# Optimization experiments

Hardware: AMD Instinct MI355X
Metric: run time of the kernel (lower is better)

Reference implementation:

```python
import jax, jax.numpy as jnp
import numpy as np

B, S, D, H = 2, 2048, 2048, 16
HD = D // H          # head dim 128
R = 64               # qk_rope_head_dim
LR = 64              # kv_low_rank_dim
FF = 2048            # ffn_dim per expert
E = 8                # num routed experts
K = 2                # top_k
ROPE_BASE = 10000.0
LN_EPS = 1e-5


def setup_inputs() -> dict:
    key = jax.random.key(0)
    ks = jax.random.split(key, 20)
    def rn(k, shape, fan_in):
        return jax.random.normal(k, shape, jnp.float32) * (1.0 / np.sqrt(fan_in))
    return {
        "hidden_states": jax.random.normal(ks[0], (B, S, D), jnp.float32),
        "position_ids": jnp.arange(S, dtype=jnp.int32)[None, :],
        # attention projections, stored [in, out]
        "Wq": rn(ks[1], (D, D), D), "Wk": rn(ks[2], (D, D), D), "Wv": rn(ks[3], (D, D), D),
        "Wkc": rn(ks[4], (HD, LR), HD), "Wvc": rn(ks[5], (HD, LR), HD),
        "Wqa": rn(ks[6], (HD, LR), HD), "Wqg": rn(ks[7], (HD, HD), HD),
        "Wov": rn(ks[8], (LR, HD), LR), "Wo": rn(ks[9], (D, D), D),
        "ln1_w": jnp.ones((D,), jnp.float32), "ln1_b": jnp.zeros((D,), jnp.float32),
        "ln2_w": jnp.ones((D,), jnp.float32), "ln2_b": jnp.zeros((D,), jnp.float32),
        # MoE
        "Wg": rn(ks[10], (D, E), D),
        "We1": rn(ks[11], (E, D, FF), D), "We2": rn(ks[12], (E, FF, D), FF), "We3": rn(ks[13], (E, D, FF), D),
        "Ws1": rn(ks[14], (D, FF), D), "Ws2": rn(ks[15], (FF, D), FF), "Ws3": rn(ks[16], (D, FF), D),
    }


def _layernorm(x, w, b):
    mu = jnp.mean(x, -1, keepdims=True)
    var = jnp.mean(jnp.square(x - mu), -1, keepdims=True)
    return (x - mu) * jax.lax.rsqrt(var + LN_EPS) * w + b


def _rotate_half(x):
    h = x.shape[-1] // 2
    return jnp.concatenate([-x[..., h:], x[..., :h]], axis=-1)


def _rope_cos_sin(position_ids, dtype):
    inv_freq = 1.0 / (ROPE_BASE ** (jnp.arange(0, R, 2, dtype=jnp.float32) / R))
    t = jnp.arange(S, dtype=jnp.float32)
    freqs = t[:, None] * inv_freq[None, :]           # [S, R/2]
    emb = jnp.concatenate([freqs, freqs], -1)        # [S, R]
    cos = jnp.cos(emb).astype(dtype)[position_ids][:, :, None, :]  # [1,S,1,R]
    sin = jnp.sin(emb).astype(dtype)[position_ids][:, :, None, :]
    return cos, sin


def reference(hidden_states, position_ids, Wq, Wk, Wv, Wkc, Wvc, Wqa, Wqg, Wov, Wo,
              ln1_w, ln1_b, ln2_w, ln2_b, Wg, We1, We2, We3, Ws1, Ws2, Ws3):
    x = _layernorm(hidden_states, ln1_w, ln1_b)
    # ---- MLA attention ----
    q = (x @ Wq).reshape(B, S, H, HD)
    k = (x @ Wk).reshape(B, S, H, HD)
    v = (x @ Wv).reshape(B, S, H, HD)
    cos, sin = _rope_cos_sin(position_ids, x.dtype)
    qr = q[..., :R] * cos + _rotate_half(q[..., :R]) * sin
    kr = k[..., :R] * cos + _rotate_half(k[..., :R]) * sin
    q = jnp.concatenate([qr, q[..., R:]], -1)
    k = jnp.concatenate([kr, k[..., R:]], -1)
    k_c = k @ Wkc                                   # [B,S,H,LR]
    v_c = v @ Wvc                                   # [B,S,H,LR]
    q_a = q @ Wqa                                   # [B,S,H,LR]
    q_gate = q @ Wqg                                # [B,S,H,HD]
    scores = jnp.einsum('bqhr,bkhr->bhqk', q_a, k_c) / np.sqrt(LR)
    attw = jax.nn.softmax(scores.astype(jnp.float32), axis=-1).astype(q.dtype)
    att_c = jnp.einsum('bhqk,bkhr->bqhr', attw, v_c)  # [B,S,H,LR]
    uplift = att_c @ Wov                              # [B,S,H,HD]
    gated = (jax.nn.silu(q_gate) * uplift).reshape(B, S, D)
    attn_out = gated @ Wo
    h = hidden_states + attn_out
    # ---- MoE with shared expert ----
    xf = _layernorm(h, ln2_w, ln2_b).reshape(-1, D)   # [T, D]
    shared = (jax.nn.silu(xf @ Ws1) * (xf @ Ws3)) @ Ws2
    logits = xf @ Wg                                  # [T, E]
    probs = jax.nn.softmax(logits.astype(jnp.float32), axis=-1)
    topw, topi = jax.lax.top_k(probs, K)
    topw = topw / jnp.sum(topw, -1, keepdims=True)
    T = xf.shape[0]
    combine = jnp.zeros((T, E), xf.dtype).at[jnp.arange(T)[:, None], topi].set(topw.astype(xf.dtype))
    h1 = jnp.einsum('td,edf->etf', xf, We1)
    h3 = jnp.einsum('td,edf->etf', xf, We3)
    eout = jnp.einsum('etf,efd->etd', jax.nn.silu(h1) * h3, We2)
    moe = shared + jnp.einsum('te,etd->td', combine, eout)
    return h + moe.reshape(B, S, D)
```

## Files before the change

kernel.cpp:

```cpp
#include <hip/hip_runtime.h>
#include <math.h>

typedef __bf16 bf16;
typedef __bf16 bf16x8 __attribute__((ext_vector_type(8)));
typedef float f32x4 __attribute__((ext_vector_type(4)));

#define B_ 2
#define S_ 2048
#define D_ 2048
#define H_ 16
#define FF_ 2048
#define E_ 8
#define T_ 4096
#define TH_ 65536
#define CAP_ 4096

#define MFMA_(a, b, c) __builtin_amdgcn_mfma_f32_16x16x32_bf16(a, b, c, 0, 0, 0)

__device__ __forceinline__ int swz(int row, int byteoff) {
  return row * 128 + (byteoff ^ ((row & 7) << 4));
}
__device__ __forceinline__ int swzf(int row, int byteoff) {
  return row * 256 + (byteoff ^ ((row & 7) << 5));
}

__device__ __forceinline__ void split2(float x, bf16& h, bf16& m) {
  h = (bf16)x;
  m = (bf16)(x - (float)h);
}

__device__ __forceinline__ void frag_split(const char* p, int off, bf16x8& r0, bf16x8& r1) {
  f32x4 u = *(const f32x4*)(p + off);
  f32x4 v = *(const f32x4*)(p + off + 16);
#pragma unroll
  for (int j = 0; j < 4; j++) { bf16 a, b; split2(u[j], a, b); r0[j] = a; r1[j] = b; }
#pragma unroll
  for (int j = 0; j < 4; j++) { bf16 a, b; split2(v[j], a, b); r0[4 + j] = a; r1[4 + j] = b; }
}

__device__ __forceinline__ f32x4 dot3(bf16x8 a0, bf16x8 a1,
                                      bf16x8 b0, bf16x8 b1, f32x4 c) {
  c = MFMA_(a0, b0, c);
  c = MFMA_(a0, b1, c);
  c = MFMA_(a1, b0, c);
  return c;
}

__device__ __forceinline__ float blk_sum(float v, float* sbuf, int tid) {
#pragma unroll
  for (int mk = 32; mk; mk >>= 1) v += __shfl_xor(v, mk);
  __syncthreads();
  if ((tid & 63) == 0) sbuf[tid >> 6] = v;
  __syncthreads();
  return sbuf[0] + sbuf[1] + sbuf[2] + sbuf[3];
}

__global__ __launch_bounds__(256) void k_transpose(const float* __restrict__ src,
                                                   bf16* __restrict__ dst, int R, int C) {
  __shared__ float tile[32][33];
  int tx = threadIdx.x, ty = threadIdx.y;
  int c0 = blockIdx.x * 32, r0 = blockIdx.y * 32;
#pragma unroll
  for (int j = 0; j < 32; j += 8) tile[ty + j][tx] = src[(size_t)(r0 + ty + j) * C + (c0 + tx)];
  __syncthreads();
#pragma unroll
  for (int j = 0; j < 32; j += 8)
    dst[(size_t)(c0 + ty + j) * R + (r0 + tx)] = (bf16)tile[tx][ty + j];
}

__global__ __launch_bounds__(256) void k_transpose32(const float* __restrict__ src,
                                                     float* __restrict__ dst, int R, int C) {
  __shared__ float tile[32][33];
  int tx = threadIdx.x, ty = threadIdx.y;
  int c0 = blockIdx.x * 32, r0 = blockIdx.y * 32;
#pragma unroll
  for (int j = 0; j < 32; j += 8) tile[ty + j][tx] = src[(size_t)(r0 + ty + j) * C + (c0 + tx)];
  __syncthreads();
#pragma unroll
  for (int j = 0; j < 32; j += 8)
    dst[(size_t)(c0 + ty + j) * R + (r0 + tx)] = tile[tx][ty + j];
}

template <int MODE>
__global__ __launch_bounds__(256) void k_transpose_moe(const float* __restrict__ W1,
                                                       const float* __restrict__ W3,
                                                       bf16* __restrict__ dstB, int eBase) {
  __shared__ float tile[32][33];
  int tx = threadIdx.x, ty = threadIdx.y;
  int z = blockIdx.z;
  const float* src;
  if (MODE == 0) src = ((z & 1) ? W3 : W1) + (size_t)(eBase + (z >> 1)) * 4194304;
  else src = W1 + (size_t)(eBase + z) * 4194304;
  bf16* dst = dstB + (size_t)z * 4194304;
  int c0 = blockIdx.x * 32, r0 = blockIdx.y * 32;
#pragma unroll
  for (int j = 0; j < 32; j += 8) tile[ty + j][tx] = src[(size_t)(r0 + ty + j) * 2048 + (c0 + tx)];
  __syncthreads();
#pragma unroll
  for (int j = 0; j < 32; j += 8)
    dst[(size_t)(c0 + ty + j) * 2048 + (r0 + tx)] = (bf16)tile[tx][ty + j];
}

__global__ __launch_bounds__(256) void k_transpose_split(const float* __restrict__ src,
                                                         bf16* __restrict__ dh, bf16* __restrict__ dl,
                                                         int R, int C) {
  __shared__ float tile[32][33];
  int tx = threadIdx.x, ty = threadIdx.y;
  int c0 = blockIdx.x * 32, r0 = blockIdx.y * 32;
#pragma unroll
  for (int j = 0; j < 32; j += 8) tile[ty + j][tx] = src[(size_t)(r0 + ty + j) * C + (c0 + tx)];
  __syncthreads();
#pragma unroll
  for (int j = 0; j < 32; j += 8) {
    float v = tile[tx][ty + j];
    bf16 h, l;
    split2(v, h, l);
    size_t o = (size_t)(c0 + ty + j) * R + (r0 + tx);
    dh[o] = h;
    dl[o] = l;
  }
}

__global__ __launch_bounds__(256) void k_tr_v32s(const float* __restrict__ vc,
                                                 bf16* __restrict__ vh, bf16* __restrict__ vl) {
  __shared__ float tile[32][33];
  int tx = threadIdx.x, ty = threadIdx.y;
  int z = blockIdx.z;
  int s0 = blockIdx.x * 32, r0 = blockIdx.y * 32;
  int b = z >> 4, h = z & 15;
#pragma unroll
  for (int j = 0; j < 32; j += 8) {
    int s = s0 + ty + j;
    tile[ty + j][tx] = vc[((size_t)((b * S_ + s) * H_ + h)) * 64 + r0 + tx];
  }
  __syncthreads();
#pragma unroll
  for (int j = 0; j < 32; j += 8) {
    int r = r0 + ty + j;
    float v = tile[tx][ty + j];
    bf16 hh, ll;
    split2(v, hh, ll);
    size_t o = ((size_t)(z * 64 + r)) * S_ + s0 + tx;
    vh[o] = hh;
    vl[o] = ll;
  }
}

__global__ __launch_bounds__(256) void k_ln32_split(const float* __restrict__ x, const float* __restrict__ w,
                                                    const float* __restrict__ bb,
                                                    bf16* __restrict__ oh, bf16* __restrict__ ol) {
  __shared__ float sbuf[4];
  int row = blockIdx.x, tid = threadIdx.x;
  const float* xr = x + (size_t)row * D_;
  float v[8];
  float s = 0.f;
#pragma unroll
  for (int j = 0; j < 8; j++) { v[j] = xr[tid + 256 * j]; s += v[j]; }
  float mu = blk_sum(s, sbuf, tid) * (1.f / D_);
  float qs = 0.f;
#pragma unroll
  for (int j = 0; j < 8; j++) { float d = v[j] - mu; qs += d * d; }
  float rs = rsqrtf(blk_sum(qs, sbuf, tid) * (1.f / D_) + 1e-5f);
#pragma unroll
  for (int j = 0; j < 8; j++) {
    int c = tid + 256 * j;
    float xn = (v[j] - mu) * rs * w[c] + bb[c];
    bf16 h, l;
    split2(xn, h, l);
    oh[(size_t)row * D_ + c] = h;
    ol[(size_t)row * D_ + c] = l;
  }
}

template <int EPI>
__global__ __launch_bounds__(256) void k_gemm32s(const bf16* __restrict__ Ah, const bf16* __restrict__ Al, int lda,
                                                 const bf16* __restrict__ Bh, const bf16* __restrict__ Bl, int ldb,
                                                 float* __restrict__ C, int ldc,
                                                 int M, int N, int Kd,
                                                 const float* __restrict__ resid) {
  __shared__ __align__(16) char Ahs[16384];
  __shared__ __align__(16) char Als[16384];
  __shared__ __align__(16) char Bhs[16384];
  __shared__ __align__(16) char Bls[16384];
  int bm = blockIdx.y * 128, bn = blockIdx.x * 128;
  int tid = threadIdx.x;
  int srow = tid >> 3, scol = (tid & 7) * 8;
  int arow[4], brow[4];
#pragma unroll
  for (int i = 0; i < 4; i++) {
    int r = bm + srow + 32 * i;
    arow[i] = r < M ? r : (M - 1);
    int q = bn + srow + 32 * i;
    brow[i] = q < N ? q : (N - 1);
  }
  f32x4 acc[4][4] = {};
  int lane = tid & 63, w = tid >> 6, g = lane >> 4, lr = lane & 15;
  int wm = (w >> 1) * 64, wn = (w & 1) * 64;
  for (int kt = 0; kt < Kd; kt += 64) {
#pragma unroll
    for (int i = 0; i < 4; i++) {
      int o = swz(srow + 32 * i, scol * 2);
      *(uint4*)(Ahs + o) = *(const uint4*)(Ah + (size_t)arow[i] * lda + kt + scol);
      *(uint4*)(Als + o) = *(const uint4*)(Al + (size_t)arow[i] * lda + kt + scol);
      *(uint4*)(Bhs + o) = *(const uint4*)(Bh + (size_t)brow[i] * ldb + kt + scol);
      *(uint4*)(Bls + o) = *(const uint4*)(Bl + (size_t)brow[i] * ldb + kt + scol);
    }
    __syncthreads();
#pragma unroll
    for (int ks = 0; ks < 2; ks++) {
      bf16x8 ah[4], al[4], bh[4], bl[4];
#pragma unroll
      for (int m = 0; m < 4; m++) {
        ah[m] = *(const bf16x8*)(Ahs + swz(wm + m * 16 + lr, ks * 64 + g * 16));
        al[m] = *(const bf16x8*)(Als + swz(wm + m * 16 + lr, ks * 64 + g * 16));
      }
#pragma unroll
      for (int n = 0; n < 4; n++) {
        bh[n] = *(const bf16x8*)(Bhs + swz(wn + n * 16 + lr, ks * 64 + g * 16));
        bl[n] = *(const bf16x8*)(Bls + swz(wn + n * 16 + lr, ks * 64 + g * 16));
      }
#pragma unroll
      for (int m = 0; m < 4; m++)
#pragma unroll
        for (int n = 0; n < 4; n++)
          acc[m][n] = dot3(ah[m], al[m], bh[n], bl[n], acc[m][n]);
    }
    __syncthreads();
  }
#pragma unroll
  for (int m = 0; m < 4; m++)
#pragma unroll
    for (int n = 0; n < 4; n++)
#pragma unroll
      for (int r = 0; r < 4; r++) {
        int row = bm + wm + m * 16 + g * 4 + r;
        int col = bn + wn + n * 16 + lr;
        if (row < M && col < N) {
          float val = acc[m][n][r];
          if (EPI == 1) val += resid[(size_t)row * ldc + col];
          C[(size_t)row * ldc + col] = val;
        }
      }
}

template <int EPI>
__global__ __launch_bounds__(256) void k_gemm32(const float* __restrict__ A, int lda,
                                                const float* __restrict__ Bt, int ldb,
                                                float* __restrict__ C, int ldc,
                                                int M, int N, int Kd,
                                                bf16* __restrict__ Ch, bf16* __restrict__ Cl) {
  __shared__ __align__(16) char As[32768];
  __shared__ __align__(16) char Bs[32768];
  int bm = blockIdx.y * 128, bn = blockIdx.x * 128;
  int tid = threadIdx.x;
  int srow = tid >> 3, scol = (tid & 7) * 8;
  int arow[4], brow[4];
#pragma unroll
  for (int i = 0; i < 4; i++) {
    int r = bm + srow + 32 * i;
    arow[i] = r < M ? r : (M - 1);
    int q = bn + srow + 32 * i;
    brow[i] = q < N ? q : (N - 1);
  }
  f32x4 acc[4][4] = {};
  int lane = tid & 63, w = tid >> 6, g = lane >> 4, lr = lane & 15;
  int wm = (w >> 1) * 64, wn = (w & 1) * 64;
  for (int kt = 0; kt < Kd; kt += 64) {
#pragma unroll
    for (int i = 0; i < 4; i++) {
      const float* pa = A + (size_t)arow[i] * lda + kt + scol;
      f32x4 va0 = *(const f32x4*)pa, va1 = *(const f32x4*)(pa + 4);
      const float* pb = Bt + (size_t)brow[i] * ldb + kt + scol;
      f32x4 vb0 = *(const f32x4*)pb, vb1 = *(const f32x4*)(pb + 4);
      int o = swzf(srow + 32 * i, scol * 4);
      *(f32x4*)(As + o) = va0;
      *(f32x4*)(As + o + 16) = va1;
      *(f32x4*)(Bs + o) = vb0;
      *(f32x4*)(Bs + o + 16) = vb1;
    }
    __syncthreads();
#pragma unroll
    for (int ks = 0; ks < 2; ks++) {
      bf16x8 a0[4], a1[4], b0[4], b1[4];
#pragma unroll
      for (int m = 0; m < 4; m++)
        frag_split(As, swzf(wm + m * 16 + lr, ks * 128 + g * 32), a0[m], a1[m]);
#pragma unroll
      for (int n = 0; n < 4; n++)
        frag_split(Bs, swzf(wn + n * 16 + lr, ks * 128 + g * 32), b0[n], b1[n]);
#pragma unroll
      for (int m = 0; m < 4; m++)
#pragma unroll
        for (int n = 0; n < 4; n++)
          acc[m][n] = dot3(a0[m], a1[m], b0[n], b1[n], acc[m][n]);
    }
    __syncthreads();
  }
#pragma unroll
  for (int m = 0; m < 4; m++)
#pragma unroll
    for (int n = 0; n < 4; n++)
#pragma unroll
      for (int r = 0; r < 4; r++) {
        int row = bm + wm + m * 16 + g * 4 + r;
        int col = bn + wn + n * 16 + lr;
        if (row < M && col < N) {
          float val = acc[m][n][r];
          if (EPI == 2) {
            bf16 h, l;
            split2(val, h, l);
            Ch[(size_t)row * ldc + col] = h;
            Cl[(size_t)row * ldc + col] = l;
          } else {
            C[(size_t)row * ldc + col] = val;
          }
        }
      }
}

__global__ __launch_bounds__(256) void k_rope32(float* __restrict__ q, float* __restrict__ k) {
  int idx = blockIdx.x * 256 + threadIdx.x;
  int i = idx & 31, rowth = idx >> 5;
  int s = (rowth >> 4) & (S_ - 1);
  size_t base = (size_t)rowth * 128;
  float freq = expf(-0.28782313662425576f * (float)i);
  float ang = (float)s * freq;
  float sn, cs;
  sincosf(ang, &sn, &cs);
  float q1 = q[base + i], q2 = q[base + i + 32];
  q[base + i] = q1 * cs - q2 * sn;
  q[base + i + 32] = q2 * cs + q1 * sn;
  float k1 = k[base + i], k2 = k[base + i + 32];
  k[base + i] = k1 * cs - k2 * sn;
  k[base + i + 32] = k2 * cs + k1 * sn;
}

__global__ __launch_bounds__(256) void k_attn32p(const bf16* __restrict__ qh, const bf16* __restrict__ ql,
                                                 const bf16* __restrict__ kh, const bf16* __restrict__ kl,
                                                 const bf16* __restrict__ vh, const bf16* __restrict__ vl,
                                                 float* __restrict__ attc) {
  __shared__ __align__(16) char L[65536];
  int qt = blockIdx.x, bh = blockIdx.y;
  int b = bh >> 4, h = bh & 15;
  int tid = threadIdx.x, lane = tid & 63, w = tid >> 6, g = lane >> 4, lr = lane & 15;
  int s0 = qt * 128;
  int srow = tid >> 3, scol = (tid & 7) * 8;
  char* Qsh = L;
  char* Qsl = L + 16384;
#pragma unroll
  for (int i = 0; i < 4; i++) {
    int row = srow + 32 * i;
    size_t goff = ((size_t)((b * S_ + s0 + row) * H_ + h)) * 64 + scol;
    int o = swz(row, scol * 2);
    *(uint4*)(Qsh + o) = *(const uint4*)(qh + goff);
    *(uint4*)(Qsl + o) = *(const uint4*)(ql + goff);
  }
  __syncthreads();
  bf16x8 qf0[2][2], qf1[2][2];
#pragma unroll
  for (int m = 0; m < 2; m++)
#pragma unroll
    for (int ks = 0; ks < 2; ks++) {
      qf0[m][ks] = *(const bf16x8*)(Qsh + swz(w * 32 + m * 16 + lr, ks * 64 + g * 16));
      qf1[m][ks] = *(const bf16x8*)(Qsl + swz(w * 32 + m * 16 + lr, ks * 64 + g * 16));
    }
  __syncthreads();
  char* Ksh = L;
  char* Ksl = L + 8192;
  char* Vsh = L + 16384;
  char* Vsl = L + 24576;
  char* Ph = L + 32768 + w * 8192;
  char* Pl = Ph + 4096;
  f32x4 acc[2][4] = {};
  float mrun[2][4], lrun[2][4];
#pragma unroll
  for (int m = 0; m < 2; m++)
#pragma unroll
    for (int r = 0; r < 4; r++) { mrun[m][r] = -1e30f; lrun[m][r] = 0.f; }
  for (int kt = 0; kt < S_; kt += 64) {
#pragma unroll
    for (int i = 0; i < 2; i++) {
      int rr = srow + 32 * i;
      size_t koff = ((size_t)((b * S_ + kt + rr) * H_ + h)) * 64 + scol;
      size_t voff = ((size_t)(bh * 64 + rr)) * S_ + kt + scol;
      int o = swz(rr, scol * 2);
      *(uint4*)(Ksh + o) = *(const uint4*)(kh + koff);
      *(uint4*)(Ksl + o) = *(const uint4*)(kl + koff);
      *(uint4*)(Vsh + o) = *(const uint4*)(vh + voff);
      *(uint4*)(Vsl + o) = *(const uint4*)(vl + voff);
    }
    __syncthreads();
    f32x4 sc[2][4] = {};
#pragma unroll
    for (int ks = 0; ks < 2; ks++) {
      bf16x8 k0[4], k1[4];
#pragma unroll
      for (int n = 0; n < 4; n++) {
        k0[n] = *(const bf16x8*)(Ksh + swz(n * 16 + lr, ks * 64 + g * 16));
        k1[n] = *(const bf16x8*)(Ksl + swz(n * 16 + lr, ks * 64 + g * 16));
      }
#pragma unroll
      for (int m = 0; m < 2; m++)
#pragma unroll
        for (int n = 0; n < 4; n++)
          sc[m][n] = dot3(qf0[m][ks], qf1[m][ks], k0[n], k1[n], sc[m][n]);
    }
#pragma unroll
    for (int m = 0; m < 2; m++)
#pragma unroll
      for (int r = 0; r < 4; r++) {
        float a0 = sc[m][0][r] * 0.125f, a1 = sc[m][1][r] * 0.125f;
        float a2 = sc[m][2][r] * 0.125f, a3 = sc[m][3][r] * 0.125f;
        float mx = fmaxf(fmaxf(a0, a1), fmaxf(a2, a3));
#pragma unroll
        for (int mk = 1; mk < 16; mk <<= 1) mx = fmaxf(mx, __shfl_xor(mx, mk));
        float mo = mrun[m][r];
        float mn = fmaxf(mo, mx);
        float f = expf(mo - mn);
        float p0 = expf(a0 - mn), p1 = expf(a1 - mn), p2 = expf(a2 - mn), p3 = expf(a3 - mn);
        int prow = m * 16 + g * 4 + r;
        bf16 h0, l0, h1, l1, h2, l2, h3, l3;
        split2(p0, h0, l0);
        split2(p1, h1, l1);
        split2(p2, h2, l2);
        split2(p3, h3, l3);
        *(bf16*)(Ph + swz(prow, lr * 2)) = h0;
        *(bf16*)(Pl + swz(prow, lr * 2)) = l0;
        *(bf16*)(Ph + swz(prow, 32 + lr * 2)) = h1;
        *(bf16*)(Pl + swz(prow, 32 + lr * 2)) = l1;
        *(bf16*)(Ph + swz(prow, 64 + lr * 2)) = h2;
        *(bf16*)(Pl + swz(prow, 64 + lr * 2)) = l2;
        *(bf16*)(Ph + swz(prow, 96 + lr * 2)) = h3;
        *(bf16*)(Pl + swz(prow, 96 + lr * 2)) = l3;
        float ps = p0 + p1 + p2 + p3;
#pragma unroll
        for (int mk = 1; mk < 16; mk <<= 1) ps += __shfl_xor(ps, mk);
        lrun[m][r] = lrun[m][r] * f + ps;
        mrun[m][r] = mn;
#pragma unroll
        for (int n = 0; n < 4; n++) acc[m][n][r] *= f;
      }
#pragma unroll
    for (int ks = 0; ks < 2; ks++) {
      bf16x8 p0f[2], p1f[2], v0f[4], v1f[4];
#pragma unroll
      for (int m = 0; m < 2; m++) {
        p0f[m] = *(const bf16x8*)(Ph + swz(m * 16 + lr, ks * 64 + g * 16));
        p1f[m] = *(const bf16x8*)(Pl + swz(m * 16 + lr, ks * 64 + g * 16));
      }
#pragma unroll
      for (int n = 0; n < 4; n++) {
        v0f[n] = *(const bf16x8*)(Vsh + swz(n * 16 + lr, ks * 64 + g * 16));
        v1f[n] = *(const bf16x8*)(Vsl + swz(n * 16 + lr, ks * 64 + g * 16));
      }
#pragma unroll
      for (int m = 0; m < 2; m++)
#pragma unroll
        for (int n = 0; n < 4; n++)
          acc[m][n] = dot3(p0f[m], p1f[m], v0f[n], v1f[n], acc[m][n]);
    }
    __syncthreads();
  }
#pragma unroll
  for (int m = 0; m < 2; m++)
#pragma unroll
    for (int n = 0; n < 4; n++)
#pragma unroll
      for (int r = 0; r < 4; r++) {
        int s = s0 + w * 32 + m * 16 + g * 4 + r;
        attc[((size_t)((b * S_ + s) * H_ + h)) * 64 + n * 16 + lr] = acc[m][n][r] / lrun[m][r];
      }
}

__global__ __launch_bounds__(256) void k_silu32_split(const float* __restrict__ a, const float* __restrict__ b,
                                                      bf16* __restrict__ ch, bf16* __restrict__ cl, long n) {
  long i = ((long)blockIdx.x * 256 + threadIdx.x) * 8;
  if (i >= n) return;
  f32x4 av0 = *(const f32x4*)(a + i), av1 = *(const f32x4*)(a + i + 4);
  f32x4 bv0 = *(const f32x4*)(b + i), bv1 = *(const f32x4*)(b + i + 4);
  bf16x8 hv, lv;
#pragma unroll
  for (int j = 0; j < 4; j++) {
    float x = av0[j];
    float g = x / (1.f + expf(-x)) * bv0[j];
    bf16 h, l;
    split2(g, h, l);
    hv[j] = h; lv[j] = l;
  }
#pragma unroll
  for (int j = 0; j < 4; j++) {
    float x = av1[j];
    float g = x / (1.f + expf(-x)) * bv1[j];
    bf16 h, l;
    split2(g, h, l);
    hv[4 + j] = h; lv[4 + j] = l;
  }
  *(bf16x8*)(ch + i) = hv;
  *(bf16x8*)(cl + i) = lv;
}

__global__ __launch_bounds__(256) void k_router(const float* __restrict__ hbuf,
                                                const float* __restrict__ w2, const float* __restrict__ b2,
                                                const float* __restrict__ Wg, bf16* __restrict__ xf,
                                                int* __restrict__ count, int* __restrict__ permg,
                                                int* __restrict__ permt, float* __restrict__ wslot) {
  __shared__ float sbuf[4];
  int t = blockIdx.x, tid = threadIdx.x;
  const float* hr = hbuf + (size_t)t * D_;
  float v[8];
  float s = 0.f;
#pragma unroll
  for (int j = 0; j < 8; j++) { v[j] = hr[tid + 256 * j]; s += v[j]; }
  float mu = blk_sum(s, sbuf, tid) * (1.f / D_);
  float qs = 0.f;
#pragma unroll
  for (int j = 0; j < 8; j++) { float d = v[j] - mu; qs += d * d; }
  float rs = rsqrtf(blk_sum(qs, sbuf, tid) * (1.f / D_) + 1e-5f);
  float le[8] = {0, 0, 0, 0, 0, 0, 0, 0};
#pragma unroll
  for (int j = 0; j < 8; j++) {
    int c = tid + 256 * j;
    float xn = (v[j] - mu) * rs * w2[c] + b2[c];
    xf[(size_t)t * D_ + c] = (bf16)xn;
    const float* wr = Wg + (size_t)c * 8;
#pragma unroll
    for (int e = 0; e < 8; e++) le[e] += xn * wr[e];
  }
#pragma unroll
  for (int e = 0; e < 8; e++) le[e] = blk_sum(le[e], sbuf, tid);
  if (tid == 0) {
    float mx = le[0];
    for (int e = 1; e < 8; e++) mx = fmaxf(mx, le[e]);
    float p[8], sum = 0.f;
    for (int e = 0; e < 8; e++) { p[e] = expf(le[e] - mx); sum += p[e]; }
    int i0 = 0;
    for (int e = 1; e < 8; e++) if (p[e] > p[i0]) i0 = e;
    int i1 = (i0 == 0) ? 1 : 0;
    for (int e = 0; e < 8; e++) if (e != i0 && p[e] > p[i1]) i1 = e;
    float inv = 1.f / (p[i0] + p[i1]);
    int pos0 = atomicAdd(&count[i0], 1);
    permg[i0 * CAP_ + pos0] = 2 * t;
    permt[i0 * CAP_ + pos0] = t;
    int pos1 = atomicAdd(&count[i1], 1);
    permg[i1 * CAP_ + pos1] = 2 * t + 1;
    permt[i1 * CAP_ + pos1] = t;
    wslot[2 * t] = p[i0] * inv;
    wslot[2 * t + 1] = p[i1] * inv;
  }
}

template <bool GATHER>
__global__ __launch_bounds__(256) void k_gemm(const bf16* __restrict__ A, int lda,
                                              const bf16* __restrict__ Bt, int ldb,
                                              bf16* __restrict__ C, int ldc, int M, int N, int Kd,
                                              const int* __restrict__ amap,
                                              const int* __restrict__ cmap,
                                              const int* __restrict__ countp) {
  int Mz = countp ? countp[0] : M;
  int bm = blockIdx.y * 128, bn = blockIdx.x * 128;
  if (bm >= Mz) return;
  __shared__ __align__(16) char As[16384];
  __shared__ __align__(16) char Bs[16384];
  int tid = threadIdx.x;
  int srow = tid >> 3, scol = (tid & 7) * 8;
  int arow[4], brow[4];
#pragma unroll
  for (int i = 0; i < 4; i++) {
    int r = bm + srow + 32 * i;
    if (GATHER) { int rc = r < Mz ? r : (Mz - 1); arow[i] = amap[rc]; }
    else { arow[i] = r < M ? r : (M - 1); }
    int bq = bn + srow + 32 * i;
    brow[i] = bq < N ? bq : (N - 1);
  }
  f32x4 acc[4][4] = {};
  int lane = tid & 63, w = tid >> 6, g = lane >> 4, lr = lane & 15;
  int wm = (w >> 1) * 64, wn = (w & 1) * 64;
  for (int kt = 0; kt < Kd; kt += 64) {
#pragma unroll
    for (int i = 0; i < 4; i++) {
      uint4 da = *(const uint4*)(A + (size_t)arow[i] * lda + kt + scol);
      *(uint4*)(As + swz(srow + 32 * i, scol * 2)) = da;
      uint4 db = *(const uint4*)(Bt + (size_t)brow[i] * ldb + kt + scol);
      *(uint4*)(Bs + swz(srow + 32 * i, scol * 2)) = db;
    }
    __syncthreads();
#pragma unroll
    for (int ks = 0; ks < 2; ks++) {
      bf16x8 af[4], bfr[4];
#pragma unroll
      for (int m = 0; m < 4; m++) af[m] = *(const bf16x8*)(As + swz(wm + m * 16 + lr, ks * 64 + g * 16));
#pragma unroll
      for (int n = 0; n < 4; n++) bfr[n] = *(const bf16x8*)(Bs + swz(wn + n * 16 + lr, ks * 64 + g * 16));
#pragma unroll
      for (int m = 0; m < 4; m++)
#pragma unroll
        for (int n = 0; n < 4; n++)
          acc[m][n] = MFMA_(af[m], bfr[n], acc[m][n]);
    }
    __syncthreads();
  }
#pragma unroll
  for (int m = 0; m < 4; m++)
#pragma unroll
    for (int n = 0; n < 4; n++)
#pragma unroll
      for (int r = 0; r < 4; r++) {
        int row = bm + wm + m * 16 + g * 4 + r;
        int col = bn + wn + n * 16 + lr;
        if (row < Mz && col < N) {
          size_t orow = cmap ? (size_t)cmap[row] : (size_t)row;
          C[orow * ldc + col] = (bf16)acc[m][n][r];
        }
      }
}

template <int MODE>
__global__ __launch_bounds__(256) void k_gemm_moe(const bf16* __restrict__ A, int lda,
                                                  const bf16* __restrict__ wteB,
                                                  bf16* __restrict__ C0, bf16* __restrict__ C1, int ldc,
                                                  int N, int Kd,
                                                  const int* __restrict__ permt, const int* __restrict__ permg,
                                                  const int* __restrict__ count, int eBase) {
  int z = blockIdx.z;
  int e;
  const int* amap;
  const int* cmap;
  bf16* C;
  if (MODE == 0) {
    e = eBase + (z >> 1);
    amap = permt + e * CAP_;
    cmap = permg + e * CAP_;
    C = (z & 1) ? C1 : C0;
  } else {
    e = eBase + z;
    amap = permg + e * CAP_;
    cmap = permg + e * CAP_;
    C = C0;
  }
  const bf16* Bt = wteB + (size_t)z * 4194304;
  int Mz = count[e];
  int bm = blockIdx.y * 128, bn = blockIdx.x * 128;
  if (bm >= Mz) return;
  __shared__ __align__(16) char As[16384];
  __shared__ __align__(16) char Bs[16384];
  int tid = threadIdx.x;
  int srow = tid >> 3, scol = (tid & 7) * 8;
  int arow[4], brow[4];
#pragma unroll
  for (int i = 0; i < 4; i++) {
    int r = bm + srow + 32 * i;
    int rc = r < Mz ? r : (Mz - 1);
    arow[i] = amap[rc];
    int bq = bn + srow + 32 * i;
    brow[i] = bq < N ? bq : (N - 1);
  }
  f32x4 acc[4][4] = {};
  int lane = tid & 63, w = tid >> 6, g = lane >> 4, lr = lane & 15;
  int wm = (w >> 1) * 64, wn = (w & 1) * 64;
  for (int kt = 0; kt < Kd; kt += 64) {
#pragma unroll
    for (int i = 0; i < 4; i++) {
      uint4 da = *(const uint4*)(A + (size_t)arow[i] * lda + kt + scol);
      *(uint4*)(As + swz(srow + 32 * i, scol * 2)) = da;
      uint4 db = *(const uint4*)(Bt + (size_t)brow[i] * 2048 + kt + scol);
      *(uint4*)(Bs + swz(srow + 32 * i, scol * 2)) = db;
    }
    __syncthreads();
#pragma unroll
    for (int ks = 0; ks < 2; ks++) {
      bf16x8 af[4], bfr[4];
#pragma unroll
      for (int m = 0; m < 4; m++) af[m] = *(const bf16x8*)(As + swz(wm + m * 16 + lr, ks * 64 + g * 16));
#pragma unroll
      for (int n = 0; n < 4; n++) bfr[n] = *(const bf16x8*)(Bs + swz(wn + n * 16 + lr, ks * 64 + g * 16));
#pragma unroll
      for (int m = 0; m < 4; m++)
#pragma unroll
        for (int n = 0; n < 4; n++)
          acc[m][n] = MFMA_(af[m], bfr[n], acc[m][n]);
    }
    __syncthreads();
  }
#pragma unroll
  for (int m = 0; m < 4; m++)
#pragma unroll
    for (int n = 0; n < 4; n++)
#pragma unroll
      for (int r = 0; r < 4; r++) {
        int row = bm + wm + m * 16 + g * 4 + r;
        int col = bn + wn + n * 16 + lr;
        if (row < Mz && col < N) {
          C[(size_t)cmap[row] * ldc + col] = (bf16)acc[m][n][r];
        }
      }
}

__global__ __launch_bounds__(256) void k_silu_mul(const bf16* __restrict__ a, const bf16* __restrict__ b,
                                                  bf16* __restrict__ c, long n) {
  long i = ((long)blockIdx.x * 256 + threadIdx.x) * 8;
  if (i >= n) return;
  bf16x8 av = *(const bf16x8*)(a + i);
  bf16x8 bv = *(const bf16x8*)(b + i);
  bf16x8 cv;
#pragma unroll
  for (int j = 0; j < 8; j++) {
    float x = (float)av[j];
    float y = (float)bv[j];
    cv[j] = (bf16)(x / (1.f + expf(-x)) * y);
  }
  *(bf16x8*)(c + i) = cv;
}

__global__ __launch_bounds__(256) void k_combine(const float* __restrict__ hbuf, const bf16* __restrict__ shr,
                                                 const bf16* __restrict__ eout, const float* __restrict__ wslot,
                                                 float* __restrict__ out) {
  long i = ((long)blockIdx.x * 256 + threadIdx.x) * 4;
  int t = (int)(i >> 11);
  int c = (int)(i & (D_ - 1));
  float w0 = wslot[2 * t], w1 = wslot[2 * t + 1];
  float4 hv = *(const float4*)(hbuf + i);
  const bf16* s4 = shr + i;
  const bf16* e0 = eout + ((size_t)(2 * t)) * D_ + c;
  const bf16* e1 = e0 + D_;
  float4 o;
  o.x = hv.x + (float)s4[0] + w0 * (float)e0[0] + w1 * (float)e1[0];
  o.y = hv.y + (float)s4[1] + w0 * (float)e0[1] + w1 * (float)e1[1];
  o.z = hv.z + (float)s4[2] + w0 * (float)e0[2] + w1 * (float)e1[2];
  o.w = hv.w + (float)s4[3] + w0 * (float)e0[3] + w1 * (float)e1[3];
  *(float4*)(out + i) = o;
}

extern "C" void kernel_launch(void* const* d_in, const int* in_sizes, int n_in, void* d_out,
                              int out_size, void* d_ws, size_t ws_size, hipStream_t stream) {
  const float* hidden = (const float*)d_in[0];
  const float* Wq = (const float*)d_in[2];
  const float* Wk = (const float*)d_in[3];
  const float* Wv = (const float*)d_in[4];
  const float* Wkc = (const float*)d_in[5];
  const float* Wvc = (const float*)d_in[6];
  const float* Wqa = (const float*)d_in[7];
  const float* Wqg = (const float*)d_in[8];
  const float* Wov = (const float*)d_in[9];
  const float* Wo = (const float*)d_in[10];
  const float* ln1w = (const float*)d_in[11];
  const float* ln1b = (const float*)d_in[12];
  const float* ln2w = (const float*)d_in[13];
  const float* ln2b = (const float*)d_in[14];
  const float* Wg = (const float*)d_in[15];
  const float* We1 = (const float*)d_in[16];
  const float* We2 = (const float*)d_in[17];
  const float* We3 = (const float*)d_in[18];
  const float* Ws1 = (const float*)d_in[19];
  const float* Ws2 = (const float*)d_in[20];
  const float* Ws3 = (const float*)d_in[21];
  float* out = (float*)d_out;
  (void)in_sizes; (void)n_in; (void)out_size;

  const size_t MB = 1ull << 20;
  char* base = (char*)d_ws;
  float* hbuf = (float*)(base);
  bf16* shr = (bf16*)(base + 32 * MB);
  int* count = (int*)(base + 48 * MB);
  int* permg = (int*)(base + 48 * MB + 4096);
  int* permt = (int*)(base + 48 * MB + 4096 + 131072);
  float* wslot = (float*)(base + 48 * MB + 4096 + 262144);
  float* wtqa32 = (float*)(base + 49 * MB);
  float* wtkc32 = (float*)(base + 49 * MB + 32768);
  float* wtvc32 = (float*)(base + 49 * MB + 65536);
  float* wtov32 = (float*)(base + 49 * MB + 98304);
  float* wtqg32 = (float*)(base + 49 * MB + 131072);
  char* A0p = base + 50 * MB;
  char* A1p = base + 82 * MB;
  char* A2p = base + 114 * MB;
  char* A3p = base + 146 * MB;
  char* A4p = base + 178 * MB;
  char* A5p = base + 210 * MB;
  if (ws_size < 242 * MB) return;

  bf16* xln_h = (bf16*)A0p;
  bf16* xln_l = (bf16*)(A0p + 16 * MB);
  bf16* wtq_h = (bf16*)A1p;
  bf16* wtq_l = (bf16*)(A1p + 8 * MB);
  bf16* wtk_h = (bf16*)(A1p + 16 * MB);
  bf16* wtk_l = (bf16*)(A1p + 24 * MB);
  bf16* wtv_h = (bf16*)A2p;
  bf16* wtv_l = (bf16*)(A2p + 8 * MB);
  float* qb = (float*)A3p;
  float* kb = (float*)A4p;
  float* vb = (float*)A5p;
  bf16* qab_h = (bf16*)A1p;
  bf16* qab_l = (bf16*)(A1p + 8 * MB);
  bf16* kcb_h = (bf16*)(A1p + 16 * MB);
  bf16* kcb_l = (bf16*)(A1p + 24 * MB);
  float* vcb = (float*)A2p;
  bf16* vct_h = (bf16*)(A2p + 16 * MB);
  bf16* vct_l = (bf16*)(A2p + 24 * MB);
  float* qgate = (float*)A0p;
  float* attc = (float*)A3p;
  bf16* wto_h = (bf16*)(A3p + 16 * MB);
  bf16* wto_l = (bf16*)(A3p + 24 * MB);
  float* uplift = (float*)A4p;
  bf16* gated_h = (bf16*)A5p;
  bf16* gated_l = (bf16*)(A5p + 16 * MB);
  bf16* xf = (bf16*)A1p;
  bf16* s1 = (bf16*)(A1p + 16 * MB);
  bf16* wts1 = (bf16*)A2p;
  bf16* wts3 = (bf16*)(A2p + 8 * MB);
  bf16* wts2 = (bf16*)(A2p + 16 * MB);
  bf16* s3 = (bf16*)A3p;
  bf16* wteB = (bf16*)A2p;
  bf16* mid1 = (bf16*)A4p;
  bf16* mid3 = (bf16*)A5p;
  bf16* midg = (bf16*)A0p;
  bf16* eout = (bf16*)A3p;

  hipMemsetAsync(count, 0, 256, stream);

  dim3 tb(32, 8);
  k_transpose_split<<<dim3(64, 64, 1), tb, 0, stream>>>(Wq, wtq_h, wtq_l, 2048, 2048);
  k_transpose_split<<<dim3(64, 64, 1), tb, 0, stream>>>(Wk, wtk_h, wtk_l, 2048, 2048);
  k_transpose_split<<<dim3(64, 64, 1), tb, 0, stream>>>(Wv, wtv_h, wtv_l, 2048, 2048);
  k_transpose32<<<dim3(2, 4, 1), tb, 0, stream>>>(Wqa, wtqa32, 128, 64);
  k_transpose32<<<dim3(2, 4, 1), tb, 0, stream>>>(Wkc, wtkc32, 128, 64);
  k_transpose32<<<dim3(2, 4, 1), tb, 0, stream>>>(Wvc, wtvc32, 128, 64);
  k_transpose32<<<dim3(4, 4, 1), tb, 0, stream>>>(Wqg, wtqg32, 128, 128);
  k_transpose32<<<dim3(4, 2, 1), tb, 0, stream>>>(Wov, wtov32, 64, 128);

  k_ln32_split<<<T_, 256, 0, stream>>>(hidden, ln1w, ln1b, xln_h, xln_l);

  k_gemm32s<0><<<dim3(16, 32, 1), 256, 0, stream>>>(xln_h, xln_l, 2048, wtq_h, wtq_l, 2048, qb, 2048, T_, 2048, 2048, nullptr);
  k_gemm32s<0><<<dim3(16, 32, 1), 256, 0, stream>>>(xln_h, xln_l, 2048, wtk_h, wtk_l, 2048, kb, 2048, T_, 2048, 2048, nullptr);
  k_gemm32s<0><<<dim3(16, 32, 1), 256, 0, stream>>>(xln_h, xln_l, 2048, wtv_h, wtv_l, 2048, vb, 2048, T_, 2048, 2048, nullptr);

  k_rope32<<<8192, 256, 0, stream>>>(qb, kb);

  k_gemm32<2><<<dim3(1, 512, 1), 256, 0, stream>>>(qb, 128, wtqa32, 128, nullptr, 64, TH_, 64, 128, qab_h, qab_l);
  k_gemm32<2><<<dim3(1, 512, 1), 256, 0, stream>>>(kb, 128, wtkc32, 128, nullptr, 64, TH_, 64, 128, kcb_h, kcb_l);
  k_gemm32<0><<<dim3(1, 512, 1), 256, 0, stream>>>(vb, 128, wtvc32, 128, vcb, 64, TH_, 64, 128, nullptr, nullptr);
  k_gemm32<0><<<dim3(1, 512, 1), 256, 0, stream>>>(qb, 128, wtqg32, 128, qgate, 128, TH_, 128, 128, nullptr, nullptr);

  k_tr_v32s<<<dim3(64, 2, 32), tb, 0, stream>>>(vcb, vct_h, vct_l);
  k_transpose_split<<<dim3(64, 64, 1), tb, 0, stream>>>(Wo, wto_h, wto_l, 2048, 2048);

  k_attn32p<<<dim3(16, 32, 1), 256, 0, stream>>>(qab_h, qab_l, kcb_h, kcb_l, vct_h, vct_l, attc);

  k_transpose<<<dim3(64, 64, 1), tb, 0, stream>>>(Ws1, wts1, 2048, 2048);
  k_transpose<<<dim3(64, 64, 1), tb, 0, stream>>>(Ws3, wts3, 2048, 2048);
  k_transpose<<<dim3(64, 64, 1), tb, 0, stream>>>(Ws2, wts2, 2048, 2048);

  k_gemm32<0><<<dim3(1, 512, 1), 256, 0, stream>>>(attc, 64, wtov32, 64, uplift, 128, TH_, 128, 64, nullptr, nullptr);
  k_silu32_split<<<4096, 256, 0, stream>>>(qgate, uplift, gated_h, gated_l, (long)TH_ * 128);
  k_gemm32s<1><<<dim3(16, 32, 1), 256, 0, stream>>>(gated_h, gated_l, 2048, wto_h, wto_l, 2048, hbuf, 2048, T_, 2048, 2048, hidden);

  k_router<<<T_, 256, 0, stream>>>(hbuf, ln2w, ln2b, Wg, xf, count, permg, permt, wslot);

  k_gemm<false><<<dim3(16, 32, 1), 256, 0, stream>>>(xf, 2048, wts1, 2048, s1, 2048, T_, 2048, 2048, nullptr, nullptr, nullptr);
  k_gemm<false><<<dim3(16, 32, 1), 256, 0, stream>>>(xf, 2048, wts3, 2048, s3, 2048, T_, 2048, 2048, nullptr, nullptr, nullptr);
  k_silu_mul<<<4096, 256, 0, stream>>>(s1, s3, s1, (long)T_ * 2048);
  k_gemm<false><<<dim3(16, 32, 1), 256, 0, stream>>>(s1, 2048, wts2, 2048, shr, 2048, T_, 2048, 2048, nullptr, nullptr, nullptr);

  for (int p = 0; p < 4; p++) {
    k_transpose_moe<0><<<dim3(64, 64, 4), tb, 0, stream>>>(We1, We3, wteB, 2 * p);
    k_gemm_moe<0><<<dim3(16, 32, 4), 256, 0, stream>>>(xf, 2048, wteB, mid1, mid3, 2048, 2048, 2048, permt, permg, count, 2 * p);
  }
  k_silu_mul<<<8192, 256, 0, stream>>>(mid1, mid3, midg, (long)2 * T_ * 2048);
  for (int q = 0; q < 2; q++) {
    k_transpose_moe<1><<<dim3(64, 64, 4), tb, 0, stream>>>(We2, nullptr, wteB, 4 * q);
    k_gemm_moe<1><<<dim3(16, 32, 4), 256, 0, stream>>>(midg, 2048, wteB, eout, nullptr, 2048, 2048, 2048, permt, permg, count, 4 * q);
  }

  k_combine<<<8192, 256, 0, stream>>>(hbuf, shr, eout, wslot, out);
}
```

Before: 1.754 ms.

## Batch same-shape launches via grid z and prioritize MFMA in attention

Folds the separate transpose and GEMM launches for Q/K/V weights, the low-rank projections and the shared-expert weights into single launches indexed by blockIdx.z. The MoE expert transposes and GEMMs now cover more experts per launch. This cuts launch count and raises per-launch parallelism, especially for the small N=64 projections. It also adds s_setprio around the MFMA loops in attention and removes the generic boundary checks in the fused QKV GEMM. The trade-off is larger workspace buffers and code specialized to fixed shapes.

```diff
diff --git a/kernel.cpp b/kernel.cpp
--- a/kernel.cpp
+++ b/kernel.cpp
@@ -55,19 +55,6 @@
   return sbuf[0] + sbuf[1] + sbuf[2] + sbuf[3];
 }
 
-__global__ __launch_bounds__(256) void k_transpose(const float* __restrict__ src,
-                                                   bf16* __restrict__ dst, int R, int C) {
-  __shared__ float tile[32][33];
-  int tx = threadIdx.x, ty = threadIdx.y;
-  int c0 = blockIdx.x * 32, r0 = blockIdx.y * 32;
-#pragma unroll
-  for (int j = 0; j < 32; j += 8) tile[ty + j][tx] = src[(size_t)(r0 + ty + j) * C + (c0 + tx)];
-  __syncthreads();
-#pragma unroll
-  for (int j = 0; j < 32; j += 8)
-    dst[(size_t)(c0 + ty + j) * R + (r0 + tx)] = (bf16)tile[tx][ty + j];
-}
-
 __global__ __launch_bounds__(256) void k_transpose32(const float* __restrict__ src,
                                                      float* __restrict__ dst, int R, int C) {
   __shared__ float tile[32][33];
@@ -79,6 +66,42 @@
 #pragma unroll
   for (int j = 0; j < 32; j += 8)
     dst[(size_t)(c0 + ty + j) * R + (r0 + tx)] = tile[tx][ty + j];
+}
+
+__global__ __launch_bounds__(256) void k_transpose32b3(const float* __restrict__ s0,
+                                                       const float* __restrict__ s1x,
+                                                       const float* __restrict__ s2,
+                                                       float* __restrict__ dbase) {
+  __shared__ float tile[32][33];
+  int z = blockIdx.z;
+  const float* src = z == 0 ? s0 : (z == 1 ? s1x : s2);
+  float* dst = dbase + (size_t)z * 8192;
+  int tx = threadIdx.x, ty = threadIdx.y;
+  int c0 = blockIdx.x * 32, r0 = blockIdx.y * 32;
+#pragma unroll
+  for (int j = 0; j < 32; j += 8) tile[ty + j][tx] = src[(size_t)(r0 + ty + j) * 64 + (c0 + tx)];
+  __syncthreads();
+#pragma unroll
+  for (int j = 0; j < 32; j += 8)
+    dst[(size_t)(c0 + ty + j) * 128 + (r0 + tx)] = tile[tx][ty + j];
+}
+
+__global__ __launch_bounds__(256) void k_transpose_sh3(const float* __restrict__ s0,
+                                                       const float* __restrict__ s1x,
+                                                       const float* __restrict__ s2,
+                                                       bf16* __restrict__ dbase) {
+  __shared__ float tile[32][33];
+  int z = blockIdx.z;
+  const float* src = z == 0 ? s0 : (z == 1 ? s1x : s2);
+  bf16* dst = dbase + (size_t)z * 4194304;
+  int tx = threadIdx.x, ty = threadIdx.y;
+  int c0 = blockIdx.x * 32, r0 = blockIdx.y * 32;
+#pragma unroll
+  for (int j = 0; j < 32; j += 8) tile[ty + j][tx] = src[(size_t)(r0 + ty + j) * 2048 + (c0 + tx)];
+  __syncthreads();
+#pragma unroll
+  for (int j = 0; j < 32; j += 8)
+    dst[(size_t)(c0 + ty + j) * 2048 + (r0 + tx)] = (bf16)tile[tx][ty + j];
 }
 
 template <int MODE>
@@ -116,6 +139,31 @@
     bf16 h, l;
     split2(v, h, l);
     size_t o = (size_t)(c0 + ty + j) * R + (r0 + tx);
+    dh[o] = h;
+    dl[o] = l;
+  }
+}
+
+__global__ __launch_bounds__(256) void k_transpose_split3(const float* __restrict__ s0,
+                                                          const float* __restrict__ s1x,
+                                                          const float* __restrict__ s2,
+                                                          bf16* __restrict__ dbase) {
+  __shared__ float tile[32][33];
+  int z = blockIdx.z;
+  const float* src = z == 0 ? s0 : (z == 1 ? s1x : s2);
+  bf16* dh = dbase + (size_t)z * 8388608;
+  bf16* dl = dh + 4194304;
+  int tx = threadIdx.x, ty = threadIdx.y;
+  int c0 = blockIdx.x * 32, r0 = blockIdx.y * 32;
+#pragma unroll
+  for (int j = 0; j < 32; j += 8) tile[ty + j][tx] = src[(size_t)(r0 + ty + j) * 2048 + (c0 + tx)];
+  __syncthreads();
+#pragma unroll
+  for (int j = 0; j < 32; j += 8) {
+    float v = tile[tx][ty + j];
+    bf16 h, l;
+    split2(v, h, l);
+    size_t o = (size_t)(c0 + ty + j) * 2048 + (r0 + tx);
     dh[o] = h;
     dl[o] = l;
   }
@@ -243,6 +291,67 @@
       }
 }
 
+__global__ __launch_bounds__(256) void k_gemm32s_qkv(const bf16* __restrict__ Ah, const bf16* __restrict__ Al,
+                                                     const bf16* __restrict__ Bhb,
+                                                     float* __restrict__ Cb) {
+  int z = blockIdx.z;
+  const bf16* Bh = Bhb + (size_t)z * 8388608;
+  const bf16* Bl = Bh + 4194304;
+  float* C = Cb + (size_t)z * 8388608;
+  __shared__ __align__(16) char Ahs[16384];
+  __shared__ __align__(16) char Als[16384];
+  __shared__ __align__(16) char Bhs[16384];
+  __shared__ __align__(16) char Bls[16384];
+  int bm = blockIdx.y * 128, bn = blockIdx.x * 128;
+  int tid = threadIdx.x;
+  int srow = tid >> 3, scol = (tid & 7) * 8;
+  f32x4 acc[4][4] = {};
+  int lane = tid & 63, w = tid >> 6, g = lane >> 4, lr = lane & 15;
+  int wm = (w >> 1) * 64, wn = (w & 1) * 64;
+  for (int kt = 0; kt < 2048; kt += 64) {
+#pragma unroll
+    for (int i = 0; i < 4; i++) {
+      int row = srow + 32 * i;
+      int o = swz(row, scol * 2);
+      *(uint4*)(Ahs + o) = *(const uint4*)(Ah + (size_t)(bm + row) * 2048 + kt + scol);
+      *(uint4*)(Als + o) = *(const uint4*)(Al + (size_t)(bm + row) * 2048 + kt + scol);
+      *(uint4*)(Bhs + o) = *(const uint4*)(Bh + (size_t)(bn + row) * 2048 + kt + scol);
+      *(uint4*)(Bls + o) = *(const uint4*)(Bl + (size_t)(bn + row) * 2048 + kt + scol);
+    }
+    __syncthreads();
+#pragma unroll
+    for (int ks = 0; ks < 2; ks++) {
+      bf16x8 ah[4], al[4], bh[4], bl[4];
+#pragma unroll
+      for (int m = 0; m < 4; m++) {
+        ah[m] = *(const bf16x8*)(Ahs + swz(wm + m * 16 + lr, ks * 64 + g * 16));
+        al[m] = *(const bf16x8*)(Als + swz(wm + m * 16 + lr, ks * 64 + g * 16));
+      }
+#pragma unroll
+      for (int n = 0; n < 4; n++) {
+        bh[n] = *(const bf16x8*)(Bhs + swz(wn + n * 16 + lr, ks * 64 + g * 16));
+        bl[n] = *(const bf16x8*)(Bls + swz(wn + n * 16 + lr, ks * 64 + g * 16));
+      }
+#pragma unroll
+      for (int m = 0; m < 4; m++)
+#pragma unroll
+        for (int n = 0; n < 4; n++)
+          acc[m][n] = dot3(ah[m], al[m], bh[n], bl[n], acc[m][n]);
+    }
+    __syncthreads();
+  }
+#pragma unroll
+  for (int m = 0; m < 4; m++)
+#pragma unroll
+    for (int n = 0; n < 4; n++)
+#pragma unroll
+      for (int r = 0; r < 4; r++) {
+        int row = bm + wm + m * 16 + g * 4 + r;
+        int col = bn + wn + n * 16 + lr;
+        C[(size_t)row * 2048 + col] = acc[m][n][r];
+      }
+}
+
 template <int EPI>
 __global__ __launch_bounds__(256) void k_gemm32(const float* __restrict__ A, int lda,
                                                 const float* __restrict__ Bt, int ldb,
@@ -305,15 +414,78 @@
         int row = bm + wm + m * 16 + g * 4 + r;
         int col = bn + wn + n * 16 + lr;
         if (row < M && col < N) {
-          float val = acc[m][n][r];
-          if (EPI == 2) {
-            bf16 h, l;
-            split2(val, h, l);
-            Ch[(size_t)row * ldc + col] = h;
-            Cl[(size_t)row * ldc + col] = l;
-          } else {
-            C[(size_t)row * ldc + col] = val;
-          }
+          C[(size_t)row * ldc + col] = acc[m][n][r];
+        }
+      }
+}
+
+__global__ __launch_bounds__(256) void k_projn64(const float* __restrict__ Ab,
+                                                 const float* __restrict__ Btb,
+                                                 bf16* __restrict__ Pb,
+                                                 float* __restrict__ Vb) {
+  int z = blockIdx.z;
+  const float* A = Ab + (size_t)z * 8388608;
+  const float* Bt = Btb + (size_t)z * 8192;
+  __shared__ __align__(16) char As[32768];
+  __shared__ __align__(16) char Bs[16384];
+  int bm = blockIdx.y * 128;
+  int tid = threadIdx.x;
+  int lane = tid & 63, w = tid >> 6, g = lane >> 4, lr = lane & 15;
+  int arowB = tid >> 2;
+  int acol = (tid & 3) * 16;
+  f32x4 acc[2][4] = {};
+  for (int kt = 0; kt < 128; kt += 64) {
+#pragma unroll
+    for (int i = 0; i < 2; i++) {
+      int row = arowB + 64 * i;
+      const float* pa = A + (size_t)(bm + row) * 128 + kt + acol;
+#pragma unroll
+      for (int j = 0; j < 4; j++)
+        *(f32x4*)(As + swzf(row, (acol + j * 4) * 4)) = *(const f32x4*)(pa + j * 4);
+    }
+    {
+      const float* pb = Bt + (size_t)arowB * 128 + kt + acol;
+#pragma unroll
+      for (int j = 0; j < 4; j++)
+        *(f32x4*)(Bs + swzf(arowB, (acol + j * 4) * 4)) = *(const f32x4*)(pb + j * 4);
+    }
+    __syncthreads();
+#pragma unroll
+    for (int ks = 0; ks < 2; ks++) {
+      bf16x8 a0[2], a1[2], b0[4], b1[4];
+#pragma unroll
+      for (int m = 0; m < 2; m++)
+        frag_split(As, swzf(w * 32 + m * 16 + lr, ks * 128 + g * 32), a0[m], a1[m]);
+#pragma unroll
+      for (int n = 0; n < 4; n++)
+        frag_split(Bs, swzf(n * 16 + lr, ks * 128 + g * 32), b0[n], b1[n]);
+#pragma unroll
+      for (int m = 0; m < 2; m++)
+#pragma unroll
+        for (int n = 0; n < 4; n++)
+          acc[m][n] = dot3(a0[m], a1[m], b0[n], b1[n], acc[m][n]);
+    }
+    __syncthreads();
+  }
+  bf16* Ph = Pb + (size_t)z * 8388608;
+  bf16* Pl = Ph + 4194304;
+#pragma unroll
+  for (int m = 0; m < 2; m++)
+#pragma unroll
+    for (int n = 0; n < 4; n++)
+#pragma unroll
+      for (int r = 0; r < 4; r++) {
+        int row = bm + w * 32 + m * 16 + g * 4 + r;
+        int col = n * 16 + lr;
+        size_t o = (size_t)row * 64 + col;
+        float val = acc[m][n][r];
+        if (z == 2) {
+          Vb[o] = val;
+        } else {
+          bf16 h, l;
+          split2(val, h, l);
+          Ph[o] = h;
+          Pl[o] = l;
         }
       }
 }
@@ -399,11 +571,13 @@
         k0[n] = *(const bf16x8*)(Ksh + swz(n * 16 + lr, ks * 64 + g * 16));
         k1[n] = *(const bf16x8*)(Ksl + swz(n * 16 + lr, ks * 64 + g * 16));
       }
+      __builtin_amdgcn_s_setprio(1);
 #pragma unroll
       for (int m = 0; m < 2; m++)
 #pragma unroll
         for (int n = 0; n < 4; n++)
           sc[m][n] = dot3(qf0[m][ks], qf1[m][ks], k0[n], k1[n], sc[m][n]);
+      __builtin_amdgcn_s_setprio(0);
     }
 #pragma unroll
     for (int m = 0; m < 2; m++)
@@ -453,11 +627,13 @@
         v0f[n] = *(const bf16x8*)(Vsh + swz(n * 16 + lr, ks * 64 + g * 16));
         v1f[n] = *(const bf16x8*)(Vsl + swz(n * 16 + lr, ks * 64 + g * 16));
       }
+      __builtin_amdgcn_s_setprio(1);
 #pragma unroll
       for (int m = 0; m < 2; m++)
 #pragma unroll
         for (int n = 0; n < 4; n++)
           acc[m][n] = dot3(p0f[m], p1f[m], v0f[n], v1f[n], acc[m][n]);
+      __builtin_amdgcn_s_setprio(0);
     }
     __syncthreads();
   }
@@ -765,8 +941,6 @@
   int* permt = (int*)(base + 48 * MB + 4096 + 131072);
   float* wslot = (float*)(base + 48 * MB + 4096 + 262144);
   float* wtqa32 = (float*)(base + 49 * MB);
-  float* wtkc32 = (float*)(base + 49 * MB + 32768);
-  float* wtvc32 = (float*)(base + 49 * MB + 65536);
   float* wtov32 = (float*)(base + 49 * MB + 98304);
   float* wtqg32 = (float*)(base + 49 * MB + 131072);
   char* A0p = base + 50 * MB;
@@ -779,12 +953,7 @@
 
   bf16* xln_h = (bf16*)A0p;
   bf16* xln_l = (bf16*)(A0p + 16 * MB);
-  bf16* wtq_h = (bf16*)A1p;
-  bf16* wtq_l = (bf16*)(A1p + 8 * MB);
-  bf16* wtk_h = (bf16*)(A1p + 16 * MB);
-  bf16* wtk_l = (bf16*)(A1p + 24 * MB);
-  bf16* wtv_h = (bf16*)A2p;
-  bf16* wtv_l = (bf16*)(A2p + 8 * MB);
+  bf16* wtqkv = (bf16*)A1p;
   float* qb = (float*)A3p;
   float* kb = (float*)A4p;
   float* vb = (float*)A5p;
@@ -808,7 +977,8 @@
   bf16* wts3 = (bf16*)(A2p + 8 * MB);
   bf16* wts2 = (bf16*)(A2p + 16 * MB);
   bf16* s3 = (bf16*)A3p;
-  bf16* wteB = (bf16*)A2p;
+  bf16* wteB_mid = (bf16*)A2p;
+  bf16* wteB_out = (bf16*)A1p;
   bf16* mid1 = (bf16*)A4p;
   bf16* mid3 = (bf16*)A5p;
   bf16* midg = (bf16*)A0p;
@@ -817,26 +987,18 @@
   hipMemsetAsync(count, 0, 256, stream);
 
   dim3 tb(32, 8);
-  k_transpose_split<<<dim3(64, 64, 1), tb, 0, stream>>>(Wq, wtq_h, wtq_l, 2048, 2048);
-  k_transpose_split<<<dim3(64, 64, 1), tb, 0, stream>>>(Wk, wtk_h, wtk_l, 2048, 2048);
-  k_transpose_split<<<dim3(64, 64, 1), tb, 0, stream>>>(Wv, wtv_h, wtv_l, 2048, 2048);
-  k_transpose32<<<dim3(2, 4, 1), tb, 0, stream>>>(Wqa, wtqa32, 128, 64);
-  k_transpose32<<<dim3(2, 4, 1), tb, 0, stream>>>(Wkc, wtkc32, 128, 64);
-  k_transpose32<<<dim3(2, 4, 1), tb, 0, stream>>>(Wvc, wtvc32, 128, 64);
+  k_transpose_split3<<<dim3(64, 64, 3), tb, 0, stream>>>(Wq, Wk, Wv, wtqkv);
+  k_transpose32b3<<<dim3(2, 4, 3), tb, 0, stream>>>(Wqa, Wkc, Wvc, wtqa32);
   k_transpose32<<<dim3(4, 4, 1), tb, 0, stream>>>(Wqg, wtqg32, 128, 128);
   k_transpose32<<<dim3(4, 2, 1), tb, 0, stream>>>(Wov, wtov32, 64, 128);
 
   k_ln32_split<<<T_, 256, 0, stream>>>(hidden, ln1w, ln1b, xln_h, xln_l);
 
-  k_gemm32s<0><<<dim3(16, 32, 1), 256, 0, stream>>>(xln_h, xln_l, 2048, wtq_h, wtq_l, 2048, qb, 2048, T_, 2048, 2048, nullptr);
-  k_gemm32s<0><<<dim3(16, 32, 1), 256, 0, stream>>>(xln_h, xln_l, 2048, wtk_h, wtk_l, 2048, kb, 2048, T_, 2048, 2048, nullptr);
-  k_gemm32s<0><<<dim3(16, 32, 1), 256, 0, stream>>>(xln_h, xln_l, 2048, wtv_h, wtv_l, 2048, vb, 2048, T_, 2048, 2048, nullptr);
+  k_gemm32s_qkv<<<dim3(16, 32, 3), 256, 0, stream>>>(xln_h, xln_l, wtqkv, qb);
 
   k_rope32<<<8192, 256, 0, stream>>>(qb, kb);
 
-  k_gemm32<2><<<dim3(1, 512, 1), 256, 0, stream>>>(qb, 128, wtqa32, 128, nullptr, 64, TH_, 64, 128, qab_h, qab_l);
-  k_gemm32<2><<<dim3(1, 512, 1), 256, 0, stream>>>(kb, 128, wtkc32, 128, nullptr, 64, TH_, 64, 128, kcb_h, kcb_l);
-  k_gemm32<0><<<dim3(1, 512, 1), 256, 0, stream>>>(vb, 128, wtvc32, 128, vcb, 64, TH_, 64, 128, nullptr, nullptr);
+  k_projn64<<<dim3(1, 512, 3), 256, 0, stream>>>(qb, wtqa32, qab_h, vcb);
   k_gemm32<0><<<dim3(1, 512, 1), 256, 0, stream>>>(qb, 128, wtqg32, 128, qgate, 128, TH_, 128, 128, nullptr, nullptr);
 
   k_tr_v32s<<<dim3(64, 2, 32), tb, 0, stream>>>(vcb, vct_h, vct_l);
@@ -844,9 +1006,7 @@
 
   k_attn32p<<<dim3(16, 32, 1), 256, 0, stream>>>(qab_h, qab_l, kcb_h, kcb_l, vct_h, vct_l, attc);
 
-  k_transpose<<<dim3(64, 64, 1), tb, 0, stream>>>(Ws1, wts1, 2048, 2048);
-  k_transpose<<<dim3(64, 64, 1), tb, 0, stream>>>(Ws3, wts3, 2048, 2048);
-  k_transpose<<<dim3(64, 64, 1), tb, 0, stream>>>(Ws2, wts2, 2048, 2048);
+  k_transpose_sh3<<<dim3(64, 64, 3), tb, 0, stream>>>(Ws1, Ws3, Ws2, wts1);
 
   k_gemm32<0><<<dim3(1, 512, 1), 256, 0, stream>>>(attc, 64, wtov32, 64, uplift, 128, TH_, 128, 64, nullptr, nullptr);
   k_silu32_split<<<4096, 256, 0, stream>>>(qgate, uplift, gated_h, gated_l, (long)TH_ * 128);
@@ -859,15 +1019,13 @@
   k_silu_mul<<<4096, 256, 0, stream>>>(s1, s3, s1, (long)T_ * 2048);
   k_gemm<false><<<dim3(16, 32, 1), 256, 0, stream>>>(s1, 2048, wts2, 2048, shr, 2048, T_, 2048, 2048, nullptr, nullptr, nullptr);
 
-  for (int p = 0; p < 4; p++) {
-    k_transpose_moe<0><<<dim3(64, 64, 4), tb, 0, stream>>>(We1, We3, wteB, 2 * p);
-    k_gemm_moe<0><<<dim3(16, 32, 4), 256, 0, stream>>>(xf, 2048, wteB, mid1, mid3, 2048, 2048, 2048, permt, permg, count, 2 * p);
+  for (int p = 0; p < 2; p++) {
+    k_transpose_moe<0><<<dim3(64, 64, 8), tb, 0, stream>>>(We1, We3, wteB_mid, 4 * p);
+    k_gemm_moe<0><<<dim3(16, 32, 8), 256, 0, stream>>>(xf, 2048, wteB_mid, mid1, mid3, 2048, 2048, 2048, permt, permg, count, 4 * p);
   }
   k_silu_mul<<<8192, 256, 0, stream>>>(mid1, mid3, midg, (long)2 * T_ * 2048);
-  for (int q = 0; q < 2; q++) {
-    k_transpose_moe<1><<<dim3(64, 64, 4), tb, 0, stream>>>(We2, nullptr, wteB, 4 * q);
-    k_gemm_moe<1><<<dim3(16, 32, 4), 256, 0, stream>>>(midg, 2048, wteB, eout, nullptr, 2048, 2048, 2048, permt, permg, count, 4 * q);
-  }
+  k_transpose_moe<1><<<dim3(64, 64, 8), tb, 0, stream>>>(We2, nullptr, wteB_out, 0);
+  k_gemm_moe<1><<<dim3(16, 32, 8), 256, 0, stream>>>(midg, 2048, wteB_out, eout, nullptr, 2048, 2048, 2048, permt, permg, count, 0);
 
   k_combine<<<8192, 256, 0, stream>>>(hbuf, shr, eout, wslot, out);
 }
```

After: 1.608 ms. 8.4% less time.
